# Performance work log

Measured on AMD Instinct MI355X. Metric: run time of the kernel, lower is better.

The kernel has to match this reference:

```python
import jax, jax.numpy as jnp
import numpy as np

DT = 0.001          # continuous-dynamics step (dt > 0 branch)
KERNEL_SIZE = 16384 # L
P, H = 1024, 256    # d_state, d_input (= d_output)


def setup_inputs() -> dict:
    key = jax.random.key(0)
    kAr, kAi, kB, kC = jax.random.split(key, 4)
    # Continuous diagonal state matrix: real part in [strong, weak] = [-0.5, -0.01] (stable),
    # imaginary part uniform in [-pi, pi] (mimics diagonal_state_space_matrix init).
    Ar = jax.random.uniform(kAr, (P,), minval=-0.5, maxval=-0.01)
    Ai = jax.random.uniform(kAi, (P,), minval=-np.pi, maxval=np.pi)
    A = jnp.stack([Ar, Ai], axis=-1).astype(jnp.float32)            # (P, 2) view_as_real
    # B, C ~ uniform disk (radius 1): scaled complex gaussians are a fine stand-in numerically.
    B = (jax.random.normal(kB, (P, H, 2)) / np.sqrt(H)).astype(jnp.float32)   # (P, H, 2)
    C = (jax.random.normal(kC, (H, P, 2)) / np.sqrt(P)).astype(jnp.float32)   # (H, P, 2)
    return {"A": A, "B": B, "C": C}


def _as_complex(x):
    return x[..., 0] + 1j * x[..., 1]


def reference(A, B, C):
    """Vandermonde SSM kernel generation (continuous dt > 0 branch).
    Returns kernel (H, L, 2) = real view of complex kernel (H, L)."""
    Ac = _as_complex(A)   # (P,) complex
    Bc = _as_complex(B)   # (P, H)
    Cc = _as_complex(C)   # (H, P)

    # ZOH-style discretization
    A_bar = jnp.exp(Ac * DT)                               # (P,)
    B_bar = ((A_bar - 1.0) / Ac)[:, None] * Bc             # (P, H)

    # Vandermonde matrix V[p, l] = A_bar[p] ** l  (complex power == exp(l * log(a)))
    powers = jnp.arange(KERNEL_SIZE, dtype=jnp.float32)    # (L,)
    V = jnp.exp(jnp.log(A_bar)[:, None] * powers[None, :]) # (P, L)

    # W[h, p] = C[h, p] * B_bar[p, h]; kernel[h, l] = sum_p W[h, p] * V[p, l]
    W = Cc * B_bar.T                                       # (H, P)
    kernel = jnp.einsum('hp,pl->hl', W, V)                 # (H, L) complex
    return jnp.stack([kernel.real, kernel.imag], axis=-1)  # (H, L, 2) float32
```

## Files before the change

### kernel.cpp

```cpp
#include <hip/hip_runtime.h>
#include <hip/hip_fp16.h>

#define P_DIM 1024
#define H_DIM 256
#define L_DIM 16384
#define DT 0.001f
#define TWOPI 6.283185307179586f
#define INV2PI 0.15915494309189535f
#define WSCALE 4096.0f
#define INV_WSCALE (1.0f / 4096.0f)
#define BM 128
#define BN 128
#define BK 64
#define NT 256

typedef _Float16 f16x8 __attribute__((ext_vector_type(8)));
typedef float f32x4 __attribute__((ext_vector_type(4)));

#define GPTR(p) (const __attribute__((address_space(1))) unsigned*)(p)
#define LPTR(p) (__attribute__((address_space(3))) unsigned*)(p)

union H2U { __half2 h; unsigned u; };

__device__ __forceinline__ float2 cmulf(float2 a, float2 b) {
    return make_float2(a.x * b.x - a.y * b.y, a.x * b.y + a.y * b.x);
}

__global__ __launch_bounds__(256)
void prep_kernel(const float* __restrict__ Ag, const float* __restrict__ Bg,
                 const float* __restrict__ Cg, __half* __restrict__ W2) {
    __shared__ float2 Bt[64][33];
    __shared__ float2 sc[64];
    const int t  = threadIdx.x;
    const int p0 = (blockIdx.x & 15) << 6;
    const int h0 = (blockIdx.x >> 4) << 5;

    if (t < 64) {
        float2 a = ((const float2*)Ag)[p0 + t];
        float er = __expf(a.x * DT);
        float s, c; __sincosf(a.y * DT, &s, &c);
        float nr = er * c - 1.f, ni = er * s;
        float inv = 1.f / (a.x * a.x + a.y * a.y);
        sc[t] = make_float2((nr * a.x + ni * a.y) * inv, (ni * a.x - nr * a.y) * inv);
    }
    #pragma unroll
    for (int i = 0; i < 8; ++i) {
        int idx = i * 256 + t, p = idx >> 5, h = idx & 31;
        Bt[p][h] = ((const float2*)Bg)[(size_t)(p0 + p) * H_DIM + h0 + h];
    }
    __syncthreads();
    #pragma unroll
    for (int i = 0; i < 8; ++i) {
        int idx = i * 256 + t, h = idx >> 6, p = idx & 63;
        float2 cc = ((const float2*)Cg)[(size_t)(h0 + h) * P_DIM + p0 + p];
        float2 s2 = sc[p], b = Bt[p][h];
        float2 tv = cmulf(cc, s2);
        float wr = (tv.x * b.x - tv.y * b.y) * WSCALE;
        float wi = (tv.x * b.y + tv.y * b.x) * WSCALE;
        ((__half2*)W2)[(size_t)(h0 + h) * P_DIM + p0 + p] =
            __float22half2_rn(make_float2(wr, wi));
    }
}

__global__ __launch_bounds__(NT, 2)
void vand_mfma_kernel(const float* __restrict__ Ag,
                      const _Float16* __restrict__ W2,
                      float* __restrict__ out) {
    __shared__ __attribute__((aligned(16))) _Float16 As[2][BM * BK];
    __shared__ __attribute__((aligned(16))) _Float16 Bs[2][BN * BK];
    __shared__ float4 Atab[P_DIM];

    const int tid  = threadIdx.x;
    const int lane = tid & 63;
    const int w    = tid >> 6;
    const int wm   = w & 1, wn = w >> 1;
    const int m0   = blockIdx.y * BM;
    const int nb   = blockIdx.x * BN;
    const int lb   = blockIdx.x * (BN / 2);

    const float2* Ag2 = (const float2*)Ag;

    #pragma unroll
    for (int i = 0; i < 4; ++i) {
        int p = tid + i * 256;
        float2 a = Ag2[p];
        float e = __expf(a.x * DT);
        float s, c; __sincosf(a.y * DT, &s, &c);
        Atab[p] = make_float4(e * c, e * s, a.x * DT, a.y * (DT * INV2PI));
    }

    f32x4 acc[4][4];
    #pragma unroll
    for (int mt = 0; mt < 4; ++mt)
        #pragma unroll
        for (int nt = 0; nt < 4; ++nt)
            acc[mt][nt] = (f32x4){0.f, 0.f, 0.f, 0.f};

    const int pl    = tid & 31;
    const int lg    = tid >> 5;
    const float l0f = (float)(lb + lg * 8);
    const int cq3   = (pl >> 2) << 3;
    const int cs    = (2 * pl) & 7;
    const int vbase = lg * 1024 + cs;

    const int goff = (lane >> 3) * 2048 + (((lane & 7) ^ (lane >> 3)) << 3);
    const _Float16* gwbase = W2 + (size_t)(m0 + (w << 5)) * 2048;
    const int ldsoff = (w << 5) * 64;

    _Float16* Acur = &As[0][0]; _Float16* Bcur = &Bs[0][0];
    _Float16* Anxt = &As[1][0]; _Float16* Bnxt = &Bs[1][0];

#define DMA_CHUNK(K0, DST)                                                        \
    {                                                                             \
        const _Float16* gw = gwbase + (K0) + goff;                                \
        _Float16* lB = (DST) + ldsoff;                                            \
        _Pragma("unroll")                                                         \
        for (int r = 0; r < 4; ++r)                                               \
            __builtin_amdgcn_global_load_lds(GPTR(gw + r * 8 * 2048),             \
                                             LPTR(lB + r * 8 * 64), 16, 0, 0);    \
    }

#define VGEN_CHUNK(K0, DST)                                                       \
    {                                                                             \
        const int pg = ((K0) >> 1) + pl;                                          \
        float4 t4 = Atab[pg];                                                     \
        float mg = __expf(t4.z * l0f);                                            \
        float x  = t4.w * l0f; x -= rintf(x);                                     \
        float s, c; __sincosf(x * TWOPI, &s, &c);                                 \
        float2 v  = make_float2(mg * c, mg * s);                                  \
        float2 ab = make_float2(t4.x, t4.y);                                      \
        _Pragma("unroll")                                                         \
        for (int j = 0; j < 8; ++j) {                                             \
            H2U u0, u1;                                                           \
            u0.h = __float22half2_rn(make_float2(v.x, -v.y));                     \
            u1.h = __float22half2_rn(make_float2(v.y, v.x));                      \
            int e0 = vbase + j * 128 + (cq3 ^ (((2 * j) & 7) << 3));              \
            int e1 = vbase + j * 128 + 64 + (cq3 ^ (((2 * j + 1) & 7) << 3));     \
            *(unsigned*)((DST) + e0) = u0.u;                                      \
            *(unsigned*)((DST) + e1) = u1.u;                                      \
            if (j < 7) v = cmulf(v, ab);                                          \
        }                                                                         \
    }

#define MFMA_HALF(KS)                                                             \
    {                                                                             \
        f16x8 af[4], bf[4];                                                       \
        const int g = (KS) * 4 + (lane >> 4);                                     \
        _Pragma("unroll")                                                         \
        for (int t = 0; t < 4; ++t) {                                             \
            int m = wm * 64 + t * 16 + (lane & 15);                               \
            af[t] = *(const f16x8*)(Acur + m * 64 + ((g ^ (m & 7)) << 3));        \
            int n = wn * 64 + t * 16 + (lane & 15);                               \
            bf[t] = *(const f16x8*)(Bcur + n * 64 + ((g ^ (n & 7)) << 3));        \
        }                                                                         \
        __builtin_amdgcn_s_setprio(1);                                            \
        _Pragma("unroll")                                                         \
        for (int mt = 0; mt < 4; ++mt)                                            \
            _Pragma("unroll")                                                     \
            for (int nt = 0; nt < 4; ++nt)                                        \
                acc[mt][nt] = __builtin_amdgcn_mfma_f32_16x16x32_f16(             \
                    af[mt], bf[nt], acc[mt][nt], 0, 0, 0);                        \
        __builtin_amdgcn_s_setprio(0);                                            \
    }

    DMA_CHUNK(0, Acur)
    __syncthreads();
    VGEN_CHUNK(0, Bcur)
    asm volatile("s_waitcnt lgkmcnt(0)" ::: "memory");
    __builtin_amdgcn_sched_barrier(0);
    __builtin_amdgcn_s_barrier();
    __builtin_amdgcn_sched_barrier(0);

    for (int kk = 0; kk < 32; ++kk) {
        if (kk < 31) {
            DMA_CHUNK((kk + 1) * BK, Anxt)
            asm volatile("s_waitcnt vmcnt(4)" ::: "memory");
        } else {
            asm volatile("s_waitcnt vmcnt(0)" ::: "memory");
        }
        __builtin_amdgcn_sched_barrier(0);
        __builtin_amdgcn_s_barrier();
        __builtin_amdgcn_sched_barrier(0);

        MFMA_HALF(0)
        if (kk < 31) {
            VGEN_CHUNK((kk + 1) * BK, Bnxt)
        }
        MFMA_HALF(1)

        asm volatile("s_waitcnt lgkmcnt(0)" ::: "memory");
        __builtin_amdgcn_sched_barrier(0);
        __builtin_amdgcn_s_barrier();
        __builtin_amdgcn_sched_barrier(0);

        _Float16* tA = Acur; Acur = Anxt; Anxt = tA;
        _Float16* tB = Bcur; Bcur = Bnxt; Bnxt = tB;
    }

    #pragma unroll
    for (int mt = 0; mt < 4; ++mt) {
        #pragma unroll
        for (int nt = 0; nt < 4; ++nt) {
            int h = m0 + wm * 64 + mt * 16 + ((lane >> 4) << 2);
            int n = nb + wn * 64 + nt * 16 + (lane & 15);
            #pragma unroll
            for (int r = 0; r < 4; ++r)
                out[(size_t)(h + r) * 32768 + n] = acc[mt][nt][r] * INV_WSCALE;
        }
    }
#undef DMA_CHUNK
#undef VGEN_CHUNK
#undef MFMA_HALF
}

extern "C" void kernel_launch(void* const* d_in, const int* in_sizes, int n_in,
                              void* d_out, int out_size, void* d_ws, size_t ws_size,
                              hipStream_t stream) {
    const float* A = (const float*)d_in[0];
    const float* B = (const float*)d_in[1];
    const float* C = (const float*)d_in[2];
    float* out = (float*)d_out;
    __half* W2 = (__half*)d_ws;

    prep_kernel<<<dim3(128), dim3(256), 0, stream>>>(A, B, C, W2);
    vand_mfma_kernel<<<dim3(L_DIM * 2 / BN, H_DIM / BM), dim3(NT), 0, stream>>>(
        A, (const _Float16*)W2, out);
}
```

Baseline: 110.8 us.

## Widen N tile to 256 with 8 waves and split V generation around MFMA clusters

Doubles the N tile to 256 columns and the block to 512 threads (8 waves), so each block covers twice as many kernel positions. Each block loads the fp16 W tile once for those positions, which halves redundant W reads per output. The main loop becomes a two-phase schedule: fragment reads, then half of the Vandermonde generation (anchor plus four power steps) interleaved with the DMA, then barriers, then the MFMA cluster. This is meant to overlap V-generation ALU work with matrix-core work. The risks are higher LDS use (about 112 KB per block), fewer blocks (256, roughly one per CU), extra barriers per iteration, and the launch-bounds attribute needing to match 512 threads.

```diff
diff --git a/kernel.cpp b/kernel.cpp
--- a/kernel.cpp
+++ b/kernel.cpp
@@ -10,9 +10,9 @@
 #define WSCALE 4096.0f
 #define INV_WSCALE (1.0f / 4096.0f)
 #define BM 128
-#define BN 128
+#define BN 256
 #define BK 64
-#define NT 256
+#define NT 512
 
 typedef _Float16 f16x8 __attribute__((ext_vector_type(8)));
 typedef float f32x4 __attribute__((ext_vector_type(4)));
@@ -81,8 +81,8 @@
     const float2* Ag2 = (const float2*)Ag;
 
     #pragma unroll
-    for (int i = 0; i < 4; ++i) {
-        int p = tid + i * 256;
+    for (int i = 0; i < 2; ++i) {
+        int p = tid + i * 512;
         float2 a = Ag2[p];
         float e = __expf(a.x * DT);
         float s, c; __sincosf(a.y * DT, &s, &c);
@@ -104,47 +104,49 @@
     const int vbase = lg * 1024 + cs;
 
     const int goff = (lane >> 3) * 2048 + (((lane & 7) ^ (lane >> 3)) << 3);
-    const _Float16* gwbase = W2 + (size_t)(m0 + (w << 5)) * 2048;
-    const int ldsoff = (w << 5) * 64;
+    const _Float16* gwbase = W2 + (size_t)(m0 + (w << 4)) * 2048;
+    const int ldsoff = (w << 4) * 64;
 
     _Float16* Acur = &As[0][0]; _Float16* Bcur = &Bs[0][0];
     _Float16* Anxt = &As[1][0]; _Float16* Bnxt = &Bs[1][0];
+
+    float2 vv, ab;
 
 #define DMA_CHUNK(K0, DST)                                                        \
     {                                                                             \
         const _Float16* gw = gwbase + (K0) + goff;                                \
         _Float16* lB = (DST) + ldsoff;                                            \
         _Pragma("unroll")                                                         \
-        for (int r = 0; r < 4; ++r)                                               \
+        for (int r = 0; r < 2; ++r)                                               \
             __builtin_amdgcn_global_load_lds(GPTR(gw + r * 8 * 2048),             \
                                              LPTR(lB + r * 8 * 64), 16, 0, 0);    \
     }
 
-#define VGEN_CHUNK(K0, DST)                                                       \
+#define VGEN_ANCHOR(K0)                                                           \
     {                                                                             \
         const int pg = ((K0) >> 1) + pl;                                          \
         float4 t4 = Atab[pg];                                                     \
         float mg = __expf(t4.z * l0f);                                            \
         float x  = t4.w * l0f; x -= rintf(x);                                     \
         float s, c; __sincosf(x * TWOPI, &s, &c);                                 \
-        float2 v  = make_float2(mg * c, mg * s);                                  \
-        float2 ab = make_float2(t4.x, t4.y);                                      \
-        _Pragma("unroll")                                                         \
-        for (int j = 0; j < 8; ++j) {                                             \
-            H2U u0, u1;                                                           \
-            u0.h = __float22half2_rn(make_float2(v.x, -v.y));                     \
-            u1.h = __float22half2_rn(make_float2(v.y, v.x));                      \
-            int e0 = vbase + j * 128 + (cq3 ^ (((2 * j) & 7) << 3));              \
-            int e1 = vbase + j * 128 + 64 + (cq3 ^ (((2 * j + 1) & 7) << 3));     \
-            *(unsigned*)((DST) + e0) = u0.u;                                      \
-            *(unsigned*)((DST) + e1) = u1.u;                                      \
-            if (j < 7) v = cmulf(v, ab);                                          \
-        }                                                                         \
-    }
-
-#define MFMA_HALF(KS)                                                             \
-    {                                                                             \
-        f16x8 af[4], bf[4];                                                       \
+        vv = make_float2(mg * c, mg * s);                                         \
+        ab = make_float2(t4.x, t4.y);                                             \
+    }
+
+#define VGEN_J(DST, J)                                                            \
+    {                                                                             \
+        H2U u0, u1;                                                               \
+        u0.h = __float22half2_rn(make_float2(vv.x, -vv.y));                       \
+        u1.h = __float22half2_rn(make_float2(vv.y, vv.x));                        \
+        int e0 = vbase + (J) * 128 + (cq3 ^ (((2 * (J)) & 7) << 3));              \
+        int e1 = vbase + (J) * 128 + 64 + (cq3 ^ (((2 * (J) + 1) & 7) << 3));     \
+        *(unsigned*)((DST) + e0) = u0.u;                                          \
+        *(unsigned*)((DST) + e1) = u1.u;                                          \
+        vv = cmulf(vv, ab);                                                       \
+    }
+
+#define FRAG_READS(KS)                                                            \
+    {                                                                             \
         const int g = (KS) * 4 + (lane >> 4);                                     \
         _Pragma("unroll")                                                         \
         for (int t = 0; t < 4; ++t) {                                             \
@@ -153,46 +155,62 @@
             int n = wn * 64 + t * 16 + (lane & 15);                               \
             bf[t] = *(const f16x8*)(Bcur + n * 64 + ((g ^ (n & 7)) << 3));        \
         }                                                                         \
-        __builtin_amdgcn_s_setprio(1);                                            \
+    }
+
+#define MFMA_CLUSTER                                                              \
+    __builtin_amdgcn_s_setprio(1);                                                \
+    _Pragma("unroll")                                                             \
+    for (int mt = 0; mt < 4; ++mt)                                                \
         _Pragma("unroll")                                                         \
-        for (int mt = 0; mt < 4; ++mt)                                            \
-            _Pragma("unroll")                                                     \
-            for (int nt = 0; nt < 4; ++nt)                                        \
-                acc[mt][nt] = __builtin_amdgcn_mfma_f32_16x16x32_f16(             \
-                    af[mt], bf[nt], acc[mt][nt], 0, 0, 0);                        \
-        __builtin_amdgcn_s_setprio(0);                                            \
-    }
+        for (int nt = 0; nt < 4; ++nt)                                            \
+            acc[mt][nt] = __builtin_amdgcn_mfma_f32_16x16x32_f16(                 \
+                af[mt], bf[nt], acc[mt][nt], 0, 0, 0);                            \
+    __builtin_amdgcn_s_setprio(0);
 
     DMA_CHUNK(0, Acur)
     __syncthreads();
-    VGEN_CHUNK(0, Bcur)
+    VGEN_ANCHOR(0)
+    VGEN_J(Bcur, 0) VGEN_J(Bcur, 1) VGEN_J(Bcur, 2) VGEN_J(Bcur, 3)
+    VGEN_J(Bcur, 4) VGEN_J(Bcur, 5) VGEN_J(Bcur, 6) VGEN_J(Bcur, 7)
     asm volatile("s_waitcnt lgkmcnt(0)" ::: "memory");
     __builtin_amdgcn_sched_barrier(0);
     __builtin_amdgcn_s_barrier();
     __builtin_amdgcn_sched_barrier(0);
 
     for (int kk = 0; kk < 32; ++kk) {
-        if (kk < 31) {
-            DMA_CHUNK((kk + 1) * BK, Anxt)
-            asm volatile("s_waitcnt vmcnt(4)" ::: "memory");
-        } else {
+        {
+            f16x8 af[4], bf[4];
+            FRAG_READS(0)
+            if (kk < 31) {
+                DMA_CHUNK((kk + 1) * BK, Anxt)
+                VGEN_ANCHOR((kk + 1) * BK)
+                VGEN_J(Bnxt, 0) VGEN_J(Bnxt, 1) VGEN_J(Bnxt, 2) VGEN_J(Bnxt, 3)
+            }
+            __builtin_amdgcn_sched_barrier(0);
+            __builtin_amdgcn_s_barrier();
+            asm volatile("s_waitcnt lgkmcnt(0)" ::: "memory");
+            __builtin_amdgcn_sched_barrier(0);
+            MFMA_CLUSTER
+            __builtin_amdgcn_sched_barrier(0);
+            __builtin_amdgcn_s_barrier();
+            __builtin_amdgcn_sched_barrier(0);
+        }
+        {
+            f16x8 af[4], bf[4];
+            FRAG_READS(1)
+            if (kk < 31) {
+                VGEN_J(Bnxt, 4) VGEN_J(Bnxt, 5) VGEN_J(Bnxt, 6) VGEN_J(Bnxt, 7)
+            }
             asm volatile("s_waitcnt vmcnt(0)" ::: "memory");
+            __builtin_amdgcn_sched_barrier(0);
+            __builtin_amdgcn_s_barrier();
+            asm volatile("s_waitcnt lgkmcnt(0)" ::: "memory");
+            __builtin_amdgcn_sched_barrier(0);
+            MFMA_CLUSTER
+            __builtin_amdgcn_sched_barrier(0);
+            __builtin_amdgcn_s_barrier();
+            __builtin_amdgcn_sched_barrier(0);
         }
-        __builtin_amdgcn_sched_barrier(0);
-        __builtin_amdgcn_s_barrier();
-        __builtin_amdgcn_sched_barrier(0);
-
-        MFMA_HALF(0)
-        if (kk < 31) {
-            VGEN_CHUNK((kk + 1) * BK, Bnxt)
-        }
-        MFMA_HALF(1)
-
-        asm volatile("s_waitcnt lgkmcnt(0)" ::: "memory");
-        __builtin_amdgcn_sched_barrier(0);
-        __builtin_amdgcn_s_barrier();
-        __builtin_amdgcn_sched_barrier(0);
-
         _Float16* tA = Acur; Acur = Anxt; Anxt = tA;
         _Float16* tB = Bcur; Bcur = Bnxt; Bnxt = tB;
     }
@@ -209,8 +227,10 @@
         }
     }
 #undef DMA_CHUNK
-#undef VGEN_CHUNK
-#undef MFMA_HALF
+#undef VGEN_ANCHOR
+#undef VGEN_J
+#undef FRAG_READS
+#undef MFMA_CLUSTER
 }
 
 extern "C" void kernel_launch(void* const* d_in, const int* in_sizes, int n_in,
```

After: 111.2 us. About the same (+0.3%).
